# Kernel optimization log

Hardware: AMD Instinct MI355X
Metric: run time of the kernel (lower is better)

## Reference

```python
import jax, jax.numpy as jnp
import numpy as np
import math

N_ENTITIES = 200000
N_ITEMS = 100000
N_REL = 40
DIM = 64
N_HEADS = 2
DK = DIM // N_HEADS
N_EDGES = 1500000
K_EDGES = 256
K_ITEMS = 100


def setup_inputs() -> dict:
    key = jax.random.key(0)
    k1, k2, k3, k4, k5, k6 = jax.random.split(key, 6)
    entity_emb = jax.random.normal(k1, (N_ENTITIES, DIM), jnp.float32) * 0.1
    W_Q = jax.random.normal(k2, (DIM, DIM), jnp.float32) * (1.0 / math.sqrt(DIM))
    relation_emb = jax.random.normal(k3, (N_REL - 1, DIM), jnp.float32) * 0.1
    edge_index = jax.random.randint(k4, (2, N_EDGES), 0, N_ENTITIES, jnp.int32)
    # edge_type in [1, N_REL-1]: code indexes relation_emb[edge_type - 1]
    edge_type = jax.random.randint(k5, (N_EDGES,), 1, N_REL, jnp.int32)
    # uniform(0,1) driving the gumbel noise -log(-log(u)); clipped away from 0
    noise_u = jax.random.uniform(k6, (N_EDGES,), jnp.float32, 1e-9, 1.0)
    return {"entity_emb": entity_emb, "W_Q": W_Q, "relation_emb": relation_emb,
            "noise_u": noise_u, "edge_index": edge_index, "edge_type": edge_type}


def reference(entity_emb, W_Q, relation_emb, noise_u, edge_index, edge_type):
    head, tail = edge_index[0], edge_index[1]
    E = edge_index.shape[1]

    # --- norm_attn_computer (AttnHGCN): per-edge multi-head attention ---
    # project once on nodes, then gather (same math as (emb[head] @ W_Q))
    proj = entity_emb @ W_Q                               # [N, D]
    q = proj[head].reshape(E, N_HEADS, DK)                # [E, H, Dk]
    k = proj[tail].reshape(E, N_HEADS, DK)                # [E, H, Dk]
    rel = relation_emb[edge_type - 1].reshape(E, N_HEADS, DK)
    attn = jnp.sum(q * k * rel, axis=-1) / math.sqrt(DK)  # [E, H]
    edge_attn_logits = attn.mean(axis=-1)                 # [E]

    # scatter_softmax over head nodes, then multiply by head degree (norm)
    seg_max = jax.lax.stop_gradient(
        jax.ops.segment_max(edge_attn_logits, head, num_segments=N_ENTITIES))
    ex = jnp.exp(edge_attn_logits - seg_max[head])
    denom = jax.ops.segment_sum(ex, head, num_segments=N_ENTITIES)
    edge_attn_score = ex / denom[head]
    deg = jax.ops.segment_sum(jnp.ones_like(edge_attn_logits), head,
                              num_segments=N_ENTITIES)
    edge_attn_score = edge_attn_score * deg[head]         # [E]

    # --- attn logit sums per item (head + tail scatter_sum), topk 100 ---
    sum_by_node = (jax.ops.segment_sum(edge_attn_logits, head, num_segments=N_ENTITIES)
                   + jax.ops.segment_sum(edge_attn_logits, tail, num_segments=N_ENTITIES))
    top_items_v, top_attn_items = jax.lax.top_k(sum_by_node[:N_ITEMS], K_ITEMS)

    # --- gumbel-noise injection + edge topk 256 ---
    noisy_score = edge_attn_score + (-jnp.log(-jnp.log(noise_u)))
    topk_v, topk_attn_edge_id = jax.lax.top_k(noisy_score, K_EDGES)

    return (edge_attn_score, topk_v, topk_attn_edge_id, top_items_v, top_attn_items)
```

## Files before the change

kernel.cpp:

```cpp
#include <hip/hip_runtime.h>

#define N_ENTITIES 200000
#define N_ITEMS    100000
#define DIM        64
#define N_EDGES    1500000
#define K_EDGES    256
#define K_ITEMS    100
#define SCALE      0.08838834764831845f

#define CAND_CAP   8192
#define NBLK3      1024
#define NB1        256
#define EPB        5860
#define BSH        6
#define NBUCK      3125
#define NSC        (NBUCK * NB1)
#define L2CAP      768

typedef unsigned long long u64;


__device__ __forceinline__ unsigned fkey(float x) {
    unsigned u = __float_as_uint(x);
    return (u & 0x80000000u) ? ~u : (u | 0x80000000u);
}
__device__ __forceinline__ float funkey(unsigned k) {
    return (k & 0x80000000u) ? __uint_as_float(k & 0x7fffffffu)
                             : __uint_as_float(~k);
}

__device__ __forceinline__ unsigned select_digit(const unsigned* __restrict__ hist,
                                                 unsigned Keff, unsigned* above) {
    unsigned cum = 0;
    int b = 255;
    for (; b > 0; --b) {
        unsigned hb = hist[b];
        if (cum + hb >= Keff) break;
        cum += hb;
    }
    *above = cum;
    return (unsigned)b;
}

__global__ __launch_bounds__(256) void proj_kernel(const float* __restrict__ emb,
                                                   const float* __restrict__ W,
                                                   float* __restrict__ proj) {
    __shared__ float part[4][16][64];
    const int t = threadIdx.x;
    const int c = t & 63;
    const int q = __builtin_amdgcn_readfirstlane(t >> 6);

    float Wreg[16];
#pragma unroll
    for (int j = 0; j < 16; ++j) Wreg[j] = W[(q * 16 + j) * 64 + c];

    const int base = blockIdx.x * 16;
    const float* erow = emb + (size_t)base * 64 + q * 16;

    float acc[16];
#pragma unroll
    for (int r = 0; r < 16; ++r) acc[r] = 0.f;
#pragma unroll
    for (int r = 0; r < 16; ++r) {
#pragma unroll
        for (int j = 0; j < 16; ++j)
            acc[r] += erow[r * 64 + j] * Wreg[j];
    }
#pragma unroll
    for (int r = 0; r < 16; ++r) part[q][r][c] = acc[r];
    __syncthreads();
#pragma unroll
    for (int it = 0; it < 4; ++it) {
        int oi = t + it * 256;
        int r = oi >> 6, cc = oi & 63;
        float s = part[0][r][cc] + part[1][r][cc] + part[2][r][cc] + part[3][r][cc];
        proj[(size_t)(base + r) * 64 + cc] = s;
    }
}

__global__ __launch_bounds__(256) void bhist_kernel(const int* __restrict__ head,
                                                    unsigned* __restrict__ off) {
    __shared__ unsigned lh[NBUCK];
    for (int k = threadIdx.x; k < NBUCK; k += 256) lh[k] = 0;
    __syncthreads();
    int base = blockIdx.x * EPB;
    int end = base + EPB; if (end > N_EDGES) end = N_EDGES;
    for (int e = base + threadIdx.x; e < end; e += 256)
        atomicAdd(&lh[(unsigned)head[e] >> BSH], 1u);
    __syncthreads();
    for (int k = threadIdx.x; k < NBUCK; k += 256)
        off[(size_t)k * NB1 + blockIdx.x] = lh[k];
}

__global__ void scanA_kernel(unsigned* __restrict__ a, unsigned* __restrict__ bsum) {
    __shared__ unsigned s[256];
    int t = threadIdx.x, i = blockIdx.x * 256 + t;
    unsigned v = a[i];
    s[t] = v;
    __syncthreads();
    for (int off = 1; off < 256; off <<= 1) {
        unsigned x = s[t];
        unsigned y = (t >= off) ? s[t - off] : 0u;
        __syncthreads();
        s[t] = x + y;
        __syncthreads();
    }
    a[i] = s[t] - v;
    if (t == 255) bsum[blockIdx.x] = s[t];
}
__global__ __launch_bounds__(256) void scanB_kernel(const unsigned* __restrict__ bsum,
                                                    unsigned* __restrict__ a) {
    __shared__ unsigned part[4];
    const int b = blockIdx.x;
    const int t = threadIdx.x;
    unsigned s = 0;
    for (int j = t; j < b; j += 256) s += bsum[j];
#pragma unroll
    for (int off = 1; off < 64; off <<= 1) s += __shfl_xor(s, off, 64);
    if ((t & 63) == 0) part[t >> 6] = s;
    __syncthreads();
    unsigned prefix = part[0] + part[1] + part[2] + part[3];
    a[b * 256 + t] += prefix;
}

__global__ __launch_bounds__(256) void bscat_kernel(const int* __restrict__ head,
                                                    const int* __restrict__ tail,
                                                    const int* __restrict__ etype,
                                                    const unsigned* __restrict__ off,
                                                    u64* __restrict__ rec2) {
    __shared__ unsigned lh[NBUCK];
    __shared__ unsigned loff[NBUCK];
    for (int k = threadIdx.x; k < NBUCK; k += 256) {
        lh[k] = 0;
        loff[k] = off[(size_t)k * NB1 + blockIdx.x];
    }
    __syncthreads();
    int base = blockIdx.x * EPB;
    int end = base + EPB; if (end > N_EDGES) end = N_EDGES;
    for (int e = base + threadIdx.x; e < end; e += 256) {
        unsigned h = (unsigned)head[e];
        unsigned bkt = h >> BSH;
        unsigned r = atomicAdd(&lh[bkt], 1u);
        u64 R = ((u64)h << 45) | ((u64)(unsigned)tail[e] << 27)
              | ((u64)(unsigned)(etype[e] - 1) << 21) | (u64)(unsigned)e;
        rec2[loff[bkt] + r] = R;
    }
}

__global__ __launch_bounds__(256) void csrnode_kernel(const u64* __restrict__ rec2,
                                                      const unsigned* __restrict__ off,
                                                      const float4* __restrict__ proj4,
                                                      const float4* __restrict__ rel4,
                                                      float* __restrict__ logits,
                                                      float2* __restrict__ nd,
                                                      float* __restrict__ sumhead,
                                                      float* __restrict__ sumI) {
    __shared__ u64 sdst[L2CAP];
    __shared__ unsigned short srank[L2CAP];
    __shared__ unsigned lh[64];
    __shared__ unsigned lscan[64];
    const int t = threadIdx.x;
    const int bkt = blockIdx.x;
    const unsigned gstart = off[(size_t)bkt * NB1];
    const unsigned gend = (bkt == NBUCK - 1) ? (unsigned)N_EDGES
                                             : off[(size_t)(bkt + 1) * NB1];
    unsigned n = gend - gstart;
    if (n > L2CAP) n = L2CAP;
    if (t < 64) lh[t] = 0;
    __syncthreads();
    for (unsigned j = t; j < n; j += 256) {
        u64 R = rec2[gstart + j];
        unsigned hl = (unsigned)(R >> 45) & 63u;
        srank[j] = (unsigned short)atomicAdd(&lh[hl], 1u);
    }
    __syncthreads();
    unsigned v0 = (t < 64) ? lh[t] : 0u;
    if (t < 64) lscan[t] = v0;
    __syncthreads();
    for (int o = 1; o < 64; o <<= 1) {
        unsigned x = 0, y = 0;
        if (t < 64) { x = lscan[t]; y = (t >= o) ? lscan[t - o] : 0u; }
        __syncthreads();
        if (t < 64) lscan[t] = x + y;
        __syncthreads();
    }
    if (t < 64) lscan[t] -= v0;
    __syncthreads();
    for (unsigned j = t; j < n; j += 256) {
        u64 R = rec2[gstart + j];
        unsigned hl = (unsigned)(R >> 45) & 63u;
        sdst[lscan[hl] + srank[j]] = R;
    }
    __syncthreads();

    const int lane = t & 63;
    const int wv = t >> 6;
    const int slot = lane >> 4, sl = lane & 15;
    for (int ln = 0; ln < 16; ++ln) {
        const int local = wv * 16 + ln;
        const int node = (bkt << 6) + local;
        const unsigned s0 = lscan[local];
        const unsigned len = lh[local];
        float4 ph = proj4[(size_t)node * 16 + sl];
        float dsum = 0.f, lsum = 0.f;
        for (unsigned k0 = 0; k0 < len; k0 += 8) {
            unsigned ka = k0 + slot, kb = ka + 4;
            bool va = (ka < len), vb = (kb < len);
            u64 Ra = sdst[s0 + (va ? ka : 0u)];
            u64 Rb = sdst[s0 + (vb ? kb : 0u)];
            unsigned ta = (unsigned)(Ra >> 27) & 0x3FFFFu, ria = ((unsigned)(Ra >> 21)) & 63u;
            unsigned tb = (unsigned)(Rb >> 27) & 0x3FFFFu, rib = ((unsigned)(Rb >> 21)) & 63u;
            unsigned ea = (unsigned)Ra & 0x1FFFFFu, eb = (unsigned)Rb & 0x1FFFFFu;
            float4 pa = proj4[(size_t)ta * 16 + sl];
            float4 qa = rel4[(size_t)ria * 16 + sl];
            float4 pb = proj4[(size_t)tb * 16 + sl];
            float4 qb = rel4[(size_t)rib * 16 + sl];
            float xa = ph.x * pa.x * qa.x + ph.y * pa.y * qa.y
                     + ph.z * pa.z * qa.z + ph.w * pa.w * qa.w;
            float xb = ph.x * pb.x * qb.x + ph.y * pb.y * qb.y
                     + ph.z * pb.z * qb.z + ph.w * pb.w * qb.w;
            xa += __shfl_xor(xa, 1, 64);  xb += __shfl_xor(xb, 1, 64);
            xa += __shfl_xor(xa, 2, 64);  xb += __shfl_xor(xb, 2, 64);
            xa += __shfl_xor(xa, 4, 64);  xb += __shfl_xor(xb, 4, 64);
            xa += __shfl_xor(xa, 8, 64);  xb += __shfl_xor(xb, 8, 64);
            if (sl == 0) {
                if (va) {
                    float lg = xa * SCALE;
                    logits[ea] = lg;
                    dsum += __expf(lg);
                    lsum += lg;
                    if (ta < N_ITEMS) atomicAdd(&sumI[ta], lg);
                }
                if (vb) {
                    float lg = xb * SCALE;
                    logits[eb] = lg;
                    dsum += __expf(lg);
                    lsum += lg;
                    if (tb < N_ITEMS) atomicAdd(&sumI[tb], lg);
                }
            }
        }
        dsum += __shfl_xor(dsum, 16, 64);
        dsum += __shfl_xor(dsum, 32, 64);
        lsum += __shfl_xor(lsum, 16, 64);
        lsum += __shfl_xor(lsum, 32, 64);
        if (lane == 0) {
            nd[node] = make_float2(dsum, (float)len);
            sumhead[node] = lsum;
        }
    }
}

__global__ __launch_bounds__(256) void edge_pass3(const float* __restrict__ logits,
                           const int* __restrict__ head,
                           const float2* __restrict__ nd, const float* __restrict__ noise_u,
                           const float* __restrict__ sumhead, const float* __restrict__ sumI,
                           float* __restrict__ out_scores, unsigned* __restrict__ keysE,
                           unsigned* __restrict__ keysI, unsigned* __restrict__ hists) {
    __shared__ unsigned hh[512];
    for (int j = threadIdx.x; j < 512; j += blockDim.x) hh[j] = 0;
    __syncthreads();
    const int stride = NBLK3 * 256;
    for (int i = blockIdx.x * blockDim.x + threadIdx.x; i < N_EDGES; i += stride) {
        float lg = logits[i];
        float2 dd = nd[head[i]];
        float score = __expf(lg) / dd.x * dd.y;
        out_scores[i] = score;
        float noise = -logf(-logf(noise_u[i]));
        unsigned k = fkey(score + noise);
        keysE[i] = k;
        atomicAdd(&hh[k >> 24], 1u);
        if (i < N_ITEMS) {
            unsigned ki = fkey(sumhead[i] + sumI[i]);
            keysI[i] = ki;
            atomicAdd(&hh[256 + (ki >> 24)], 1u);
        }
    }
    __syncthreads();
    for (int j = threadIdx.x; j < 512; j += blockDim.x) {
        unsigned v = hh[j];
        if (v) atomicAdd(&hists[j], v);
    }
}

__global__ void collect_kernel(const unsigned* __restrict__ keysE,
                               const unsigned* __restrict__ keysI,
                               const unsigned* __restrict__ hists,
                               unsigned* __restrict__ counters, unsigned* __restrict__ cand) {
    const int y = blockIdx.y;
    const unsigned* keys = y ? keysI : keysE;
    const int n = y ? N_ITEMS : N_EDGES;
    const unsigned K = y ? K_ITEMS : K_EDGES;
    const unsigned* H = hists + (size_t)y * 256;
    unsigned aboveA;
    unsigned binA = select_digit(H, K, &aboveA);
    const unsigned T = binA << 24;
    unsigned* cd = cand + (size_t)y * 2 * CAND_CAP;

    int i = blockIdx.x * blockDim.x + threadIdx.x;
    int stride = gridDim.x * blockDim.x;
    for (; i < n; i += stride) {
        unsigned k = keys[i];
        if (k >= T) {
            unsigned p = atomicAdd(&counters[y], 1u);
            if (p < (unsigned)CAND_CAP) { cd[2 * p] = k; cd[2 * p + 1] = (unsigned)i; }
        }
    }
}

__global__ void final_topk_kernel(const unsigned* __restrict__ cand,
                                  const unsigned* __restrict__ counters,
                                  float* __restrict__ out_topkv, float* __restrict__ out_topki,
                                  float* __restrict__ out_itemv, float* __restrict__ out_itemi) {
    __shared__ unsigned sk[CAND_CAP];
    __shared__ unsigned si[CAND_CAP];
    const int y = blockIdx.x;
    const int K = y ? K_ITEMS : K_EDGES;
    float* outv = y ? out_itemv : out_topkv;
    float* outi = y ? out_itemi : out_topki;
    const unsigned* cd = cand + (size_t)y * 2 * CAND_CAP;
    unsigned m = counters[y];
    if (m > (unsigned)CAND_CAP) m = CAND_CAP;
    for (unsigned i = threadIdx.x; i < m; i += blockDim.x) {
        sk[i] = cd[2 * i];
        si[i] = cd[2 * i + 1];
    }
    __syncthreads();
    for (unsigned i = threadIdx.x; i < m; i += blockDim.x) {
        unsigned ki = sk[i], xi = si[i];
        int r = 0;
        for (unsigned j = 0; j < m; ++j) {
            unsigned kj = sk[j];
            if (kj > ki || (kj == ki && si[j] < xi)) r++;
        }
        if (r < K) {
            outv[r] = funkey(ki);
            outi[r] = (float)xi;
        }
    }
}

extern "C" void kernel_launch(void* const* d_in, const int* in_sizes, int n_in,
                              void* d_out, int out_size, void* d_ws, size_t ws_size,
                              hipStream_t stream) {
    (void)in_sizes; (void)n_in; (void)out_size; (void)ws_size;
    const float* emb    = (const float*)d_in[0];
    const float* W      = (const float*)d_in[1];
    const float* rel    = (const float*)d_in[2];
    const float* noise  = (const float*)d_in[3];
    const int*   eidx   = (const int*)d_in[4];
    const int*   etype  = (const int*)d_in[5];
    const int* head = eidx;
    const int* tail = eidx + N_EDGES;

    float* out        = (float*)d_out;
    float* out_scores = out;
    float* out_topkv  = out + N_EDGES;
    float* out_topki  = out + N_EDGES + K_EDGES;
    float* out_itemv  = out + N_EDGES + 2 * K_EDGES;
    float* out_itemi  = out + N_EDGES + 2 * K_EDGES + K_ITEMS;

    float* ws = (float*)d_ws;
    size_t o = 0;
    float*    proj    = ws + o;               o += (size_t)N_ENTITIES * DIM;
    unsigned* off     = (unsigned*)(ws + o);  o += NSC;
    unsigned* bsum    = (unsigned*)(ws + o);  o += 3200;
    u64*      rec2    = (u64*)(ws + o);       o += 2 * (size_t)N_EDGES;
    unsigned* keysE   = (unsigned*)rec2;
    unsigned* keysI   = keysE + N_EDGES;
    float*    logits  = ws + o;               o += N_EDGES;
    float2*   nd      = (float2*)(ws + o);    o += 2 * (size_t)N_ENTITIES;
    float*    sumhead = ws + o;               o += N_ENTITIES;
    float*    sumI    = ws + o;               o += N_ITEMS;
    unsigned* hists   = (unsigned*)(ws + o);  o += 512;
    unsigned* counters= (unsigned*)(ws + o);  o += 2;
    unsigned* cand    = (unsigned*)(ws + o);  o += 2 * 2 * CAND_CAP;

    hipMemsetAsync(sumI, 0, ((size_t)N_ITEMS + 512 + 2) * 4, stream);
    hipLaunchKernelGGL(proj_kernel, dim3(12500), dim3(256), 0, stream, emb, W, proj);
    hipLaunchKernelGGL(bhist_kernel, dim3(NB1), dim3(256), 0, stream, head, off);
    hipLaunchKernelGGL(scanA_kernel, dim3(NSC / 256), dim3(256), 0, stream, off, bsum);
    hipLaunchKernelGGL(scanB_kernel, dim3(NSC / 256), dim3(256), 0, stream, bsum, off);
    hipLaunchKernelGGL(bscat_kernel, dim3(NB1), dim3(256), 0, stream,
                       head, tail, etype, off, rec2);
    hipLaunchKernelGGL(csrnode_kernel, dim3(NBUCK), dim3(256), 0, stream,
                       rec2, off, (const float4*)proj, (const float4*)rel,
                       logits, nd, sumhead, sumI);
    hipLaunchKernelGGL(edge_pass3, dim3(NBLK3), dim3(256), 0, stream,
                       logits, head, nd, noise, sumhead, sumI,
                       out_scores, keysE, keysI, hists);
    hipLaunchKernelGGL(collect_kernel, dim3(512, 2), dim3(256), 0, stream,
                       keysE, keysI, hists, counters, cand);
    hipLaunchKernelGGL(final_topk_kernel, dim3(2), dim3(1024), 0, stream,
                       cand, counters, out_topkv, out_topki, out_itemv, out_itemi);
}
```

Before: 437.2 us.

## Fuse projection with head histogram and widen CSR buckets to 256 nodes

New measurement: 431.0 us. About the same (-1.4%).

```diff
diff --git a/kernel.cpp b/kernel.cpp
--- a/kernel.cpp
+++ b/kernel.cpp
@@ -12,10 +12,11 @@
 #define NBLK3      1024
 #define NB1        256
 #define EPB        5860
-#define BSH        6
-#define NBUCK      3125
+#define BSH        8
+#define NBUCK      782
 #define NSC        (NBUCK * NB1)
-#define L2CAP      768
+#define L2CAP      2816
+#define PROJB      12500
 
 typedef unsigned long long u64;
 
@@ -42,11 +43,29 @@
     return (unsigned)b;
 }
 
-__global__ __launch_bounds__(256) void proj_kernel(const float* __restrict__ emb,
-                                                   const float* __restrict__ W,
-                                                   float* __restrict__ proj) {
+__global__ __launch_bounds__(256) void proj_bhist_kernel(const float* __restrict__ emb,
+                                                         const float* __restrict__ W,
+                                                         float* __restrict__ proj,
+                                                         const int* __restrict__ head,
+                                                         unsigned* __restrict__ off) {
     __shared__ float part[4][16][64];
     const int t = threadIdx.x;
+
+    if (blockIdx.x >= PROJB) {
+        unsigned* lh = (unsigned*)&part[0][0][0];
+        const int vb = blockIdx.x - PROJB;
+        for (int k = t; k < NBUCK; k += 256) lh[k] = 0;
+        __syncthreads();
+        int base = vb * EPB;
+        int end = base + EPB; if (end > N_EDGES) end = N_EDGES;
+        for (int e = base + t; e < end; e += 256)
+            atomicAdd(&lh[(unsigned)head[e] >> BSH], 1u);
+        __syncthreads();
+        for (int k = t; k < NBUCK; k += 256)
+            off[(size_t)k * NB1 + vb] = lh[k];
+        return;
+    }
+
     const int c = t & 63;
     const int q = __builtin_amdgcn_readfirstlane(t >> 6);
 
@@ -76,20 +95,6 @@
         float s = part[0][r][cc] + part[1][r][cc] + part[2][r][cc] + part[3][r][cc];
         proj[(size_t)(base + r) * 64 + cc] = s;
     }
-}
-
-__global__ __launch_bounds__(256) void bhist_kernel(const int* __restrict__ head,
-                                                    unsigned* __restrict__ off) {
-    __shared__ unsigned lh[NBUCK];
-    for (int k = threadIdx.x; k < NBUCK; k += 256) lh[k] = 0;
-    __syncthreads();
-    int base = blockIdx.x * EPB;
-    int end = base + EPB; if (end > N_EDGES) end = N_EDGES;
-    for (int e = base + threadIdx.x; e < end; e += 256)
-        atomicAdd(&lh[(unsigned)head[e] >> BSH], 1u);
-    __syncthreads();
-    for (int k = threadIdx.x; k < NBUCK; k += 256)
-        off[(size_t)k * NB1 + blockIdx.x] = lh[k];
 }
 
 __global__ void scanA_kernel(unsigned* __restrict__ a, unsigned* __restrict__ bsum) {
@@ -157,8 +162,8 @@
                                                       float* __restrict__ sumI) {
     __shared__ u64 sdst[L2CAP];
     __shared__ unsigned short srank[L2CAP];
-    __shared__ unsigned lh[64];
-    __shared__ unsigned lscan[64];
+    __shared__ unsigned lh[256];
+    __shared__ unsigned lscan[256];
     const int t = threadIdx.x;
     const int bkt = blockIdx.x;
     const unsigned gstart = off[(size_t)bkt * NB1];
@@ -166,29 +171,31 @@
                                              : off[(size_t)(bkt + 1) * NB1];
     unsigned n = gend - gstart;
     if (n > L2CAP) n = L2CAP;
-    if (t < 64) lh[t] = 0;
+    lh[t] = 0;
     __syncthreads();
     for (unsigned j = t; j < n; j += 256) {
         u64 R = rec2[gstart + j];
-        unsigned hl = (unsigned)(R >> 45) & 63u;
+        unsigned hl = (unsigned)(R >> 45) & 255u;
         srank[j] = (unsigned short)atomicAdd(&lh[hl], 1u);
     }
     __syncthreads();
-    unsigned v0 = (t < 64) ? lh[t] : 0u;
-    if (t < 64) lscan[t] = v0;
-    __syncthreads();
-    for (int o = 1; o < 64; o <<= 1) {
-        unsigned x = 0, y = 0;
-        if (t < 64) { x = lscan[t]; y = (t >= o) ? lscan[t - o] : 0u; }
-        __syncthreads();
-        if (t < 64) lscan[t] = x + y;
-        __syncthreads();
-    }
-    if (t < 64) lscan[t] -= v0;
+    unsigned v0 = lh[t];
+    lscan[t] = v0;
+    __syncthreads();
+    for (int o = 1; o < 256; o <<= 1) {
+        unsigned x = lscan[t];
+        unsigned y = (t >= o) ? lscan[t - o] : 0u;
+        __syncthreads();
+        lscan[t] = x + y;
+        __syncthreads();
+    }
+    unsigned excl = lscan[t] - v0;
+    __syncthreads();
+    lscan[t] = excl;
     __syncthreads();
     for (unsigned j = t; j < n; j += 256) {
         u64 R = rec2[gstart + j];
-        unsigned hl = (unsigned)(R >> 45) & 63u;
+        unsigned hl = (unsigned)(R >> 45) & 255u;
         sdst[lscan[hl] + srank[j]] = R;
     }
     __syncthreads();
@@ -196,9 +203,10 @@
     const int lane = t & 63;
     const int wv = t >> 6;
     const int slot = lane >> 4, sl = lane & 15;
-    for (int ln = 0; ln < 16; ++ln) {
-        const int local = wv * 16 + ln;
-        const int node = (bkt << 6) + local;
+    for (int ln = 0; ln < 64; ++ln) {
+        const int local = wv * 64 + ln;
+        const int node = (bkt << BSH) + local;
+        if (node >= N_ENTITIES) break;
         const unsigned s0 = lscan[local];
         const unsigned len = lh[local];
         float4 ph = proj4[(size_t)node * 16 + sl];
@@ -364,7 +372,7 @@
     size_t o = 0;
     float*    proj    = ws + o;               o += (size_t)N_ENTITIES * DIM;
     unsigned* off     = (unsigned*)(ws + o);  o += NSC;
-    unsigned* bsum    = (unsigned*)(ws + o);  o += 3200;
+    unsigned* bsum    = (unsigned*)(ws + o);  o += 1024;
     u64*      rec2    = (u64*)(ws + o);       o += 2 * (size_t)N_EDGES;
     unsigned* keysE   = (unsigned*)rec2;
     unsigned* keysI   = keysE + N_EDGES;
@@ -377,8 +385,8 @@
     unsigned* cand    = (unsigned*)(ws + o);  o += 2 * 2 * CAND_CAP;
 
     hipMemsetAsync(sumI, 0, ((size_t)N_ITEMS + 512 + 2) * 4, stream);
-    hipLaunchKernelGGL(proj_kernel, dim3(12500), dim3(256), 0, stream, emb, W, proj);
-    hipLaunchKernelGGL(bhist_kernel, dim3(NB1), dim3(256), 0, stream, head, off);
+    hipLaunchKernelGGL(proj_bhist_kernel, dim3(PROJB + NB1), dim3(256), 0, stream,
+                       emb, W, proj, head, off);
     hipLaunchKernelGGL(scanA_kernel, dim3(NSC / 256), dim3(256), 0, stream, off, bsum);
     hipLaunchKernelGGL(scanB_kernel, dim3(NSC / 256), dim3(256), 0, stream, bsum, off);
     hipLaunchKernelGGL(bscat_kernel, dim3(NB1), dim3(256), 0, stream,
```
